# Kernel tuning notes

Hardware: AMD Instinct MI355X
Metric: run time of the kernel (lower is better)

The kernel has to match this reference:

```python
import jax, jax.numpy as jnp
import numpy as np
from jax.ops import segment_sum

N_NODES = 50000
N_EDGES = 800000
IN_DIM, HID_DIM, OUT_DIM = 128, 256, 128


def _glorot(key, shape):
    lim = np.sqrt(6.0 / (shape[0] + shape[1]))
    return jax.random.uniform(key, shape, jnp.float32, -lim, lim)


def setup_inputs() -> dict:
    key = jax.random.key(0)
    ks = jax.random.split(key, 4)
    x = jax.random.normal(ks[0], (N_NODES, IN_DIM), jnp.float32)
    edge_index = jax.random.randint(ks[1], (2, N_EDGES), 0, N_NODES, jnp.int64)
    W1 = _glorot(ks[2], (IN_DIM, HID_DIM))
    b1 = jnp.zeros((HID_DIM,), jnp.float32)
    W2 = _glorot(ks[3], (HID_DIM, OUT_DIM))
    b2 = jnp.zeros((OUT_DIM,), jnp.float32)
    return {"x": x, "edge_index": edge_index, "W1": W1, "b1": b1, "W2": W2, "b2": b2}


def gcn_conv(x, W, b, src, dst, n_nodes):
    # PyG GCNConv: x' = D^{-1/2} (A + I) D^{-1/2} (x W) + b
    h = x @ W  # [N, F_out]
    deg = segment_sum(jnp.ones_like(src, dtype=h.dtype), dst, num_segments=n_nodes) + 1.0  # +1 self loop
    dinv = jax.lax.rsqrt(deg)  # [N]
    norm = dinv[src] * dinv[dst]  # per-edge norm [E]
    msg = h[src] * norm[:, None]  # [E, F_out]
    agg = segment_sum(msg, dst, num_segments=n_nodes)
    agg = agg + h * (dinv * dinv)[:, None]  # self-loop term: norm_ii = dinv_i^2
    return agg + b


def reference(x, edge_index, W1, b1, W2, b2):
    src, dst = edge_index[0], edge_index[1]
    h = gcn_conv(x, W1, b1, src, dst, N_NODES)
    h = jax.nn.relu(h)
    out = gcn_conv(h, W2, b2, src, dst, N_NODES)
    return out
```

## Files before the change

kernel.cpp:

```cpp
#include <hip/hip_runtime.h>

#define N_NODES 50000
#define N_EDGES 800000
#define IN_DIM  128
#define HID_DIM 256
#define OUT_DIM 128
#define BUCKET_CAP 64
#define NCOARSE 196
#define CHUNK 4000
#define NBLK1 200
#define SEGCAP 64
#define AXLD 136

typedef __attribute__((ext_vector_type(8))) short short8;
typedef __attribute__((ext_vector_type(4))) float f32x4;

__device__ inline ushort f2b(float f) {
    union { float f; unsigned u; } v; v.f = f;
    return (ushort)((v.u + 0x7FFFu + ((v.u >> 16) & 1u)) >> 16);
}
__device__ inline float b2f(ushort h) {
    union { unsigned u; float f; } v; v.u = ((unsigned)h) << 16;
    return v.f;
}
__device__ inline float2 u2f2(unsigned u) {
    float2 r; r.x = b2f((ushort)(u & 0xFFFFu)); r.y = b2f((ushort)(u >> 16)); return r;
}
__device__ inline void fma2(float2& a, const float2 v, float n) {
    a.x += v.x * n; a.y += v.y * n;
}


__global__ __launch_bounds__(256) void prep_kernel(const float* __restrict__ x,
                                                   const float* __restrict__ W1,
                                                   const float* __restrict__ W2,
                                                   const int* __restrict__ src,
                                                   const int* __restrict__ dst,
                                                   ushort* __restrict__ xb,
                                                   ushort* __restrict__ w1t,
                                                   ushort* __restrict__ w2t,
                                                   int* __restrict__ bcnt,
                                                   int* __restrict__ binbuf) {
    __shared__ int vals[CHUNK];
    __shared__ ushort lpos[CHUNK];
    __shared__ unsigned char lbin[CHUNK];
    __shared__ int hist[NCOARSE];
    const int b = blockIdx.x;
    const int t = threadIdx.x;
    if (b < 6250) {
        int i = b * 256 + t;
        float4 v = ((const float4*)x)[i];
        ushort4 o; o.x = f2b(v.x); o.y = f2b(v.y); o.z = f2b(v.z); o.w = f2b(v.w);
        ((ushort4*)xb)[i] = o;
    } else if (b < 6506) {
        int i = (b - 6250) * 256 + t;
        if (i < 32768) {
            int n = i >> 7, k = i & 127;
            w1t[i] = f2b(W1[k * HID_DIM + n]);
        } else {
            int j = i - 32768;
            int n = j >> 8, k = j & 255;
            w2t[j] = f2b(W2[k * OUT_DIM + n]);
        }
    } else {
        const int blk = b - 6506;
        const int e0 = blk * CHUNK;
        for (int i = t; i < NCOARSE; i += 256) hist[i] = 0;
        __syncthreads();
        for (int i = t; i < CHUNK; i += 256) {
            int s = src[e0 + i], d = dst[e0 + i];
            int bin = d >> 8;
            vals[i] = (s << 8) | (d & 255);
            lbin[i] = (unsigned char)bin;
            lpos[i] = (ushort)atomicAdd(&hist[bin], 1);
        }
        __syncthreads();
        for (int i = t; i < NCOARSE; i += 256) {
            int h = hist[i]; if (h > SEGCAP) h = SEGCAP;
            bcnt[i * NBLK1 + blk] = h;
        }
        for (int i = t; i < CHUNK; i += 256) {
            int bin = lbin[i];
            int p = lpos[i];
            if (p < SEGCAP) binbuf[((size_t)bin * NBLK1 + blk) * SEGCAP + p] = vals[i];
        }
    }
}


__global__ __launch_bounds__(256) void binpass2_kernel(const int* __restrict__ bcnt,
                                                       const int* __restrict__ binbuf,
                                                       int* __restrict__ cnt,
                                                       float* __restrict__ dinv,
                                                       int* __restrict__ bucket) {
    __shared__ int lcnt[256];
    __shared__ int lm[NBLK1];
    __shared__ int lbuck[256 * BUCKET_CAP];
    const int bin = blockIdx.x;
    const int t = threadIdx.x;
    lcnt[t] = 0;
    if (t < NBLK1) lm[t] = bcnt[bin * NBLK1 + t];
    __syncthreads();
    const int* bb = binbuf + (size_t)bin * NBLK1 * SEGCAP;
    for (int f = t; f < NBLK1 * SEGCAP; f += 256) {
        int blk = f >> 6;
        int sl = f & 63;
        if (sl < lm[blk]) {
            int v = bb[f];
            int dl = v & 255;
            int pos = atomicAdd(&lcnt[dl], 1);
            if (pos < BUCKET_CAP) lbuck[dl * BUCKET_CAP + pos] = v >> 8;
        }
    }
    __syncthreads();
    const int node0 = bin * 256;
    int node = node0 + t;
    if (node < N_NODES) {
        int c = lcnt[t] > BUCKET_CAP ? BUCKET_CAP : lcnt[t];
        cnt[node] = c;
        dinv[node] = rsqrtf((float)c + 1.0f);
    }
    int nvalid = N_NODES - node0; if (nvalid > 256) nvalid = 256;
    if (nvalid <= 0) return;
    int total4 = (nvalid * BUCKET_CAP) >> 2;
    int4* d4 = (int4*)(bucket + (size_t)node0 * BUCKET_CAP);
    const int4* s4 = (const int4*)lbuck;
    for (int j = t; j < total4; j += 256) d4[j] = s4[j];
}


__global__ __launch_bounds__(256) void gg1_kernel(const int* __restrict__ cnt,
                                                  const int* __restrict__ bucket,
                                                  const float* __restrict__ dinv,
                                                  const ushort* __restrict__ xb,
                                                  const ushort* __restrict__ w1t,
                                                  const float* __restrict__ b1,
                                                  ushort* __restrict__ Hb) {
    __shared__ ushort axs[16 * AXLD];
    const int row0 = blockIdx.x * 16;
    const int wv = threadIdx.x >> 6;
    const int lane = threadIdx.x & 63;

    for (int j = 0; j < 4; ++j) {
        const int lr = wv * 4 + j;
        const int node = row0 + lr;
        const int n = cnt[node];
        const float dd = dinv[node];
        int sv = 0; float nv = 0.f;
        if (lane < n) { sv = bucket[node * BUCKET_CAP + lane]; nv = dinv[sv] * dd; }
        float2 self = u2f2(((const unsigned*)(xb + (size_t)node * IN_DIM))[lane]);
        float sd = dd * dd;
        float2 acc[8];
        acc[0] = {self.x * sd, self.y * sd};
#pragma unroll
        for (int k = 1; k < 8; ++k) acc[k] = {0.f, 0.f};
        const int nr = (n + 7) & ~7;
        for (int i = 0; i < nr; i += 8) {
            int s[8]; float nm[8]; unsigned u[8];
#pragma unroll
            for (int k = 0; k < 8; ++k) { s[k] = __shfl(sv, i + k); nm[k] = __shfl(nv, i + k); }
#pragma unroll
            for (int k = 0; k < 8; ++k) u[k] = ((const unsigned*)(xb + (size_t)s[k] * IN_DIM))[lane];
#pragma unroll
            for (int k = 0; k < 8; ++k) fma2(acc[k], u2f2(u[k]), nm[k]);
        }
#pragma unroll
        for (int k = 1; k < 8; ++k) { acc[0].x += acc[k].x; acc[0].y += acc[k].y; }
        unsigned o = (unsigned)f2b(acc[0].x) | ((unsigned)f2b(acc[0].y) << 16);
        ((unsigned*)(axs + lr * AXLD))[lane] = o;
    }
    __syncthreads();

    const int l15 = lane & 15, q = lane >> 4;
    f32x4 acc4[4] = {{0.f, 0.f, 0.f, 0.f}, {0.f, 0.f, 0.f, 0.f},
                     {0.f, 0.f, 0.f, 0.f}, {0.f, 0.f, 0.f, 0.f}};
    const ushort* abase = axs + l15 * AXLD + q * 8;
#pragma unroll
    for (int kb = 0; kb < 4; ++kb) {
        short8 a = *(const short8*)(abase + kb * 32);
#pragma unroll
        for (int t = 0; t < 4; ++t) {
            int col = wv * 64 + t * 16 + l15;
            short8 bfr = *(const short8*)(w1t + (size_t)col * IN_DIM + kb * 32 + q * 8);
            acc4[t] = __builtin_amdgcn_mfma_f32_16x16x32_bf16(a, bfr, acc4[t], 0, 0, 0);
        }
    }
#pragma unroll
    for (int t = 0; t < 4; ++t) {
        int col = wv * 64 + t * 16 + l15;
        float bias = b1[col];
#pragma unroll
        for (int r = 0; r < 4; ++r) {
            int row = row0 + q * 4 + r;
            float v = acc4[t][r] + bias;
            Hb[(size_t)row * HID_DIM + col] = f2b(v > 0.f ? v : 0.f);
        }
    }
}


__global__ __launch_bounds__(256) void gemm2_mfma(const ushort* __restrict__ Hb,
                                                  const ushort* __restrict__ w2t,
                                                  ushort* __restrict__ h2b) {
    const int row0 = blockIdx.x * 16;
    const int wv = threadIdx.x >> 6;
    const int lane = threadIdx.x & 63;
    const int l15 = lane & 15, q = lane >> 4;
    f32x4 acc[2] = {{0.f, 0.f, 0.f, 0.f}, {0.f, 0.f, 0.f, 0.f}};
    const ushort* abase = Hb + (size_t)(row0 + l15) * HID_DIM + q * 8;
#pragma unroll
    for (int kb = 0; kb < 8; ++kb) {
        short8 a = *(const short8*)(abase + kb * 32);
#pragma unroll
        for (int t = 0; t < 2; ++t) {
            int col = wv * 32 + t * 16 + l15;
            short8 b = *(const short8*)(w2t + (size_t)col * HID_DIM + kb * 32 + q * 8);
            acc[t] = __builtin_amdgcn_mfma_f32_16x16x32_bf16(a, b, acc[t], 0, 0, 0);
        }
    }
#pragma unroll
    for (int t = 0; t < 2; ++t) {
        int col = wv * 32 + t * 16 + l15;
#pragma unroll
        for (int r = 0; r < 4; ++r) {
            int row = row0 + q * 4 + r;
            h2b[(size_t)row * OUT_DIM + col] = f2b(acc[t][r]);
        }
    }
}


__global__ __launch_bounds__(256) void gather2_kernel(const int* __restrict__ cnt,
                                                      const int* __restrict__ bucket,
                                                      const float* __restrict__ dinv,
                                                      const ushort* __restrict__ h2b,
                                                      const float* __restrict__ b2,
                                                      float* __restrict__ out) {
    const int w = blockIdx.x * 4 + (threadIdx.x >> 6);
    const int lane = threadIdx.x & 63;
    const int n = cnt[w];
    const float dd = dinv[w];
    int sv = 0; float nv = 0.f;
    if (lane < n) { sv = bucket[w * BUCKET_CAP + lane]; nv = dinv[sv] * dd; }

    float2 bb = ((const float2*)b2)[lane];
    float2 self = u2f2(((const unsigned*)(h2b + (size_t)w * OUT_DIM))[lane]);
    float sd = dd * dd;
    float2 acc[8];
    acc[0] = {self.x * sd + bb.x, self.y * sd + bb.y};
#pragma unroll
    for (int j = 1; j < 8; ++j) acc[j] = {0.f, 0.f};

    const int nr = (n + 7) & ~7;
    for (int i = 0; i < nr; i += 8) {
        int s[8]; float nm[8]; unsigned u[8];
#pragma unroll
        for (int j = 0; j < 8; ++j) { s[j] = __shfl(sv, i + j); nm[j] = __shfl(nv, i + j); }
#pragma unroll
        for (int j = 0; j < 8; ++j) u[j] = ((const unsigned*)(h2b + (size_t)s[j] * OUT_DIM))[lane];
#pragma unroll
        for (int j = 0; j < 8; ++j) fma2(acc[j], u2f2(u[j]), nm[j]);
    }
#pragma unroll
    for (int j = 1; j < 8; ++j) { acc[0].x += acc[j].x; acc[0].y += acc[j].y; }
    ((float2*)(out + (size_t)w * OUT_DIM))[lane] = acc[0];
}

extern "C" void kernel_launch(void* const* d_in, const int* in_sizes, int n_in,
                              void* d_out, int out_size, void* d_ws, size_t ws_size,
                              hipStream_t stream) {
    const float* x  = (const float*)d_in[0];
    const int*   ei = (const int*)d_in[1];
    const float* W1 = (const float*)d_in[2];
    const float* b1 = (const float*)d_in[3];
    const float* W2 = (const float*)d_in[4];
    const float* b2 = (const float*)d_in[5];
    float* out = (float*)d_out;

    const int* src = ei;
    const int* dst = ei + N_EDGES;

    char* ws = (char*)d_ws;
    int*    bcnt   = (int*)(ws);
    int*    cnt    = (int*)(ws + 160000);
    float*  dinv   = (float*)(ws + 360000);
    int*    bucket = (int*)(ws + 560000);
    int*    binbuf = (int*)(ws + 13360000);
    ushort* xb     = (ushort*)(ws + 23395200);
    ushort* w1t    = (ushort*)(ws + 36195200);
    ushort* w2t    = (ushort*)(ws + 36260736);
    ushort* Hb     = (ushort*)(ws + 36326272);
    ushort* h2b    = (ushort*)(ws + 61926272);

    prep_kernel<<<6706, 256, 0, stream>>>(x, W1, W2, src, dst, xb, w1t, w2t, bcnt, binbuf);
    binpass2_kernel<<<NCOARSE, 256, 0, stream>>>(bcnt, binbuf, cnt, dinv, bucket);

    gg1_kernel<<<N_NODES / 16, 256, 0, stream>>>(cnt, bucket, dinv, xb, w1t, b1, Hb);

    gemm2_mfma<<<N_NODES / 16, 256, 0, stream>>>(Hb, w2t, h2b);
    gather2_kernel<<<N_NODES / 4, 256, 0, stream>>>(cnt, bucket, dinv, h2b, b2, out);
}
```

Before: 251.3 us.

## Split layer-1 gather from GEMM, fuse both GEMMs, and widen gather loads

The fused gather+GEMM1 kernel is split into a standalone gather kernel that writes the aggregated bf16 features. A new kernel fuses GEMM1 (with bias and ReLU) and GEMM2, keeping the hidden activations in LDS instead of writing the 256-wide H matrix to global memory and reading it back. Both gather kernels now use 16-byte uint4 loads, with four lane groups each handling a different neighbor, followed by a cross-group shuffle reduction. The cost is an extra global round trip for the 128-wide aggregated input and more shuffle work per edge.

```diff
diff --git a/kernel.cpp b/kernel.cpp
--- a/kernel.cpp
+++ b/kernel.cpp
@@ -10,7 +10,7 @@
 #define CHUNK 4000
 #define NBLK1 200
 #define SEGCAP 64
-#define AXLD 136
+#define HLD 264
 
 typedef __attribute__((ext_vector_type(8))) short short8;
 typedef __attribute__((ext_vector_type(4))) float f32x4;
@@ -26,8 +26,15 @@
 __device__ inline float2 u2f2(unsigned u) {
     float2 r; r.x = b2f((ushort)(u & 0xFFFFu)); r.y = b2f((ushort)(u >> 16)); return r;
 }
-__device__ inline void fma2(float2& a, const float2 v, float n) {
-    a.x += v.x * n; a.y += v.y * n;
+__device__ inline unsigned f2u2(float a, float b) {
+    return (unsigned)f2b(a) | ((unsigned)f2b(b) << 16);
+}
+__device__ inline void fma8(float2* acc, uint4 u, float n) {
+    float2 v0 = u2f2(u.x), v1 = u2f2(u.y), v2 = u2f2(u.z), v3 = u2f2(u.w);
+    acc[0].x += v0.x * n; acc[0].y += v0.y * n;
+    acc[1].x += v1.x * n; acc[1].y += v1.y * n;
+    acc[2].x += v2.x * n; acc[2].y += v2.y * n;
+    acc[3].x += v3.x * n; acc[3].y += v3.y * n;
 }
 
 
@@ -129,93 +136,103 @@
 }
 
 
-__global__ __launch_bounds__(256) void gg1_kernel(const int* __restrict__ cnt,
-                                                  const int* __restrict__ bucket,
-                                                  const float* __restrict__ dinv,
-                                                  const ushort* __restrict__ xb,
-                                                  const ushort* __restrict__ w1t,
-                                                  const float* __restrict__ b1,
-                                                  ushort* __restrict__ Hb) {
-    __shared__ ushort axs[16 * AXLD];
-    const int row0 = blockIdx.x * 16;
-    const int wv = threadIdx.x >> 6;
+__global__ __launch_bounds__(256) void gather0_kernel(const int* __restrict__ cnt,
+                                                      const int* __restrict__ bucket,
+                                                      const float* __restrict__ dinv,
+                                                      const ushort* __restrict__ xb,
+                                                      ushort* __restrict__ aggxb) {
+    const int w = blockIdx.x * 4 + (threadIdx.x >> 6);
     const int lane = threadIdx.x & 63;
-
+    const int grp = lane >> 4, sub = lane & 15;
+    const int n = cnt[w];
+    const float dd = dinv[w];
+    int sv = 0; float nv = 0.f;
+    if (lane < n) { sv = bucket[w * BUCKET_CAP + lane]; nv = dinv[sv] * dd; }
+
+    float2 acc[4];
+    if (grp == 0) {
+        uint4 su = ((const uint4*)(xb + (size_t)w * IN_DIM))[sub];
+        float sd = dd * dd;
+        acc[0] = u2f2(su.x); acc[1] = u2f2(su.y); acc[2] = u2f2(su.z); acc[3] = u2f2(su.w);
+#pragma unroll
+        for (int j = 0; j < 4; ++j) { acc[j].x *= sd; acc[j].y *= sd; }
+    } else {
+#pragma unroll
+        for (int j = 0; j < 4; ++j) acc[j] = {0.f, 0.f};
+    }
+
+    const int nr = (n + 15) & ~15;
+    for (int i = 0; i < nr; i += 16) {
+        int s0 = __shfl(sv, i + grp),      s1 = __shfl(sv, i + 4 + grp);
+        int s2 = __shfl(sv, i + 8 + grp),  s3 = __shfl(sv, i + 12 + grp);
+        float n0 = __shfl(nv, i + grp),     n1 = __shfl(nv, i + 4 + grp);
+        float n2 = __shfl(nv, i + 8 + grp), n3 = __shfl(nv, i + 12 + grp);
+        uint4 u0 = ((const uint4*)(xb + (size_t)s0 * IN_DIM))[sub];
+        uint4 u1 = ((const uint4*)(xb + (size_t)s1 * IN_DIM))[sub];
+        uint4 u2 = ((const uint4*)(xb + (size_t)s2 * IN_DIM))[sub];
+        uint4 u3 = ((const uint4*)(xb + (size_t)s3 * IN_DIM))[sub];
+        fma8(acc, u0, n0); fma8(acc, u1, n1); fma8(acc, u2, n2); fma8(acc, u3, n3);
+    }
+#pragma unroll
     for (int j = 0; j < 4; ++j) {
-        const int lr = wv * 4 + j;
-        const int node = row0 + lr;
-        const int n = cnt[node];
-        const float dd = dinv[node];
-        int sv = 0; float nv = 0.f;
-        if (lane < n) { sv = bucket[node * BUCKET_CAP + lane]; nv = dinv[sv] * dd; }
-        float2 self = u2f2(((const unsigned*)(xb + (size_t)node * IN_DIM))[lane]);
-        float sd = dd * dd;
-        float2 acc[8];
-        acc[0] = {self.x * sd, self.y * sd};
-#pragma unroll
-        for (int k = 1; k < 8; ++k) acc[k] = {0.f, 0.f};
-        const int nr = (n + 7) & ~7;
-        for (int i = 0; i < nr; i += 8) {
-            int s[8]; float nm[8]; unsigned u[8];
-#pragma unroll
-            for (int k = 0; k < 8; ++k) { s[k] = __shfl(sv, i + k); nm[k] = __shfl(nv, i + k); }
-#pragma unroll
-            for (int k = 0; k < 8; ++k) u[k] = ((const unsigned*)(xb + (size_t)s[k] * IN_DIM))[lane];
-#pragma unroll
-            for (int k = 0; k < 8; ++k) fma2(acc[k], u2f2(u[k]), nm[k]);
-        }
-#pragma unroll
-        for (int k = 1; k < 8; ++k) { acc[0].x += acc[k].x; acc[0].y += acc[k].y; }
-        unsigned o = (unsigned)f2b(acc[0].x) | ((unsigned)f2b(acc[0].y) << 16);
-        ((unsigned*)(axs + lr * AXLD))[lane] = o;
-    }
-    __syncthreads();
-
-    const int l15 = lane & 15, q = lane >> 4;
-    f32x4 acc4[4] = {{0.f, 0.f, 0.f, 0.f}, {0.f, 0.f, 0.f, 0.f},
-                     {0.f, 0.f, 0.f, 0.f}, {0.f, 0.f, 0.f, 0.f}};
-    const ushort* abase = axs + l15 * AXLD + q * 8;
-#pragma unroll
-    for (int kb = 0; kb < 4; ++kb) {
-        short8 a = *(const short8*)(abase + kb * 32);
-#pragma unroll
-        for (int t = 0; t < 4; ++t) {
-            int col = wv * 64 + t * 16 + l15;
-            short8 bfr = *(const short8*)(w1t + (size_t)col * IN_DIM + kb * 32 + q * 8);
-            acc4[t] = __builtin_amdgcn_mfma_f32_16x16x32_bf16(a, bfr, acc4[t], 0, 0, 0);
-        }
-    }
-#pragma unroll
-    for (int t = 0; t < 4; ++t) {
-        int col = wv * 64 + t * 16 + l15;
-        float bias = b1[col];
-#pragma unroll
-        for (int r = 0; r < 4; ++r) {
-            int row = row0 + q * 4 + r;
-            float v = acc4[t][r] + bias;
-            Hb[(size_t)row * HID_DIM + col] = f2b(v > 0.f ? v : 0.f);
-        }
-    }
-}
-
-
-__global__ __launch_bounds__(256) void gemm2_mfma(const ushort* __restrict__ Hb,
-                                                  const ushort* __restrict__ w2t,
-                                                  ushort* __restrict__ h2b) {
+        acc[j].x += __shfl_down(acc[j].x, 32); acc[j].y += __shfl_down(acc[j].y, 32);
+        acc[j].x += __shfl_down(acc[j].x, 16); acc[j].y += __shfl_down(acc[j].y, 16);
+    }
+    if (lane < 16) {
+        uint4 o = {f2u2(acc[0].x, acc[0].y), f2u2(acc[1].x, acc[1].y),
+                   f2u2(acc[2].x, acc[2].y), f2u2(acc[3].x, acc[3].y)};
+        ((uint4*)(aggxb + (size_t)w * IN_DIM))[sub] = o;
+    }
+}
+
+
+__global__ __launch_bounds__(256) void gemm12_mfma(const ushort* __restrict__ aggxb,
+                                                   const ushort* __restrict__ w1t,
+                                                   const float* __restrict__ b1,
+                                                   const ushort* __restrict__ w2t,
+                                                   ushort* __restrict__ h2b) {
+    __shared__ ushort Hs[16 * HLD];
     const int row0 = blockIdx.x * 16;
     const int wv = threadIdx.x >> 6;
     const int lane = threadIdx.x & 63;
     const int l15 = lane & 15, q = lane >> 4;
-    f32x4 acc[2] = {{0.f, 0.f, 0.f, 0.f}, {0.f, 0.f, 0.f, 0.f}};
-    const ushort* abase = Hb + (size_t)(row0 + l15) * HID_DIM + q * 8;
+
+    f32x4 acc1[4] = {{0.f, 0.f, 0.f, 0.f}, {0.f, 0.f, 0.f, 0.f},
+                     {0.f, 0.f, 0.f, 0.f}, {0.f, 0.f, 0.f, 0.f}};
+    const ushort* abase = aggxb + (size_t)(row0 + l15) * IN_DIM + q * 8;
+#pragma unroll
+    for (int kb = 0; kb < 4; ++kb) {
+        short8 a = *(const short8*)(abase + kb * 32);
+#pragma unroll
+        for (int t = 0; t < 4; ++t) {
+            int col = wv * 64 + t * 16 + l15;
+            short8 bfr = *(const short8*)(w1t + (size_t)col * IN_DIM + kb * 32 + q * 8);
+            acc1[t] = __builtin_amdgcn_mfma_f32_16x16x32_bf16(a, bfr, acc1[t], 0, 0, 0);
+        }
+    }
+#pragma unroll
+    for (int t = 0; t < 4; ++t) {
+        int col = wv * 64 + t * 16 + l15;
+        float bias = b1[col];
+#pragma unroll
+        for (int r = 0; r < 4; ++r) {
+            int row = q * 4 + r;
+            float v = acc1[t][r] + bias;
+            Hs[row * HLD + col] = f2b(v > 0.f ? v : 0.f);
+        }
+    }
+    __syncthreads();
+
+    f32x4 acc2[2] = {{0.f, 0.f, 0.f, 0.f}, {0.f, 0.f, 0.f, 0.f}};
+    const ushort* hbase = Hs + l15 * HLD + q * 8;
 #pragma unroll
     for (int kb = 0; kb < 8; ++kb) {
-        short8 a = *(const short8*)(abase + kb * 32);
+        short8 a = *(const short8*)(hbase + kb * 32);
 #pragma unroll
         for (int t = 0; t < 2; ++t) {
             int col = wv * 32 + t * 16 + l15;
-            short8 b = *(const short8*)(w2t + (size_t)col * HID_DIM + kb * 32 + q * 8);
-            acc[t] = __builtin_amdgcn_mfma_f32_16x16x32_bf16(a, b, acc[t], 0, 0, 0);
+            short8 bfr = *(const short8*)(w2t + (size_t)col * HID_DIM + kb * 32 + q * 8);
+            acc2[t] = __builtin_amdgcn_mfma_f32_16x16x32_bf16(a, bfr, acc2[t], 0, 0, 0);
         }
     }
 #pragma unroll
@@ -224,7 +241,7 @@
 #pragma unroll
         for (int r = 0; r < 4; ++r) {
             int row = row0 + q * 4 + r;
-            h2b[(size_t)row * OUT_DIM + col] = f2b(acc[t][r]);
+            h2b[(size_t)row * OUT_DIM + col] = f2b(acc2[t][r]);
         }
     }
 }
@@ -238,32 +255,50 @@
                                                       float* __restrict__ out) {
     const int w = blockIdx.x * 4 + (threadIdx.x >> 6);
     const int lane = threadIdx.x & 63;
+    const int grp = lane >> 4, sub = lane & 15;
     const int n = cnt[w];
     const float dd = dinv[w];
     int sv = 0; float nv = 0.f;
     if (lane < n) { sv = bucket[w * BUCKET_CAP + lane]; nv = dinv[sv] * dd; }
 
-    float2 bb = ((const float2*)b2)[lane];
-    float2 self = u2f2(((const unsigned*)(h2b + (size_t)w * OUT_DIM))[lane]);
-    float sd = dd * dd;
-    float2 acc[8];
-    acc[0] = {self.x * sd + bb.x, self.y * sd + bb.y};
-#pragma unroll
-    for (int j = 1; j < 8; ++j) acc[j] = {0.f, 0.f};
-
-    const int nr = (n + 7) & ~7;
-    for (int i = 0; i < nr; i += 8) {
-        int s[8]; float nm[8]; unsigned u[8];
-#pragma unroll
-        for (int j = 0; j < 8; ++j) { s[j] = __shfl(sv, i + j); nm[j] = __shfl(nv, i + j); }
-#pragma unroll
-        for (int j = 0; j < 8; ++j) u[j] = ((const unsigned*)(h2b + (size_t)s[j] * OUT_DIM))[lane];
-#pragma unroll
-        for (int j = 0; j < 8; ++j) fma2(acc[j], u2f2(u[j]), nm[j]);
-    }
-#pragma unroll
-    for (int j = 1; j < 8; ++j) { acc[0].x += acc[j].x; acc[0].y += acc[j].y; }
-    ((float2*)(out + (size_t)w * OUT_DIM))[lane] = acc[0];
+    float2 acc[4];
+    if (grp == 0) {
+        uint4 su = ((const uint4*)(h2b + (size_t)w * OUT_DIM))[sub];
+        float sd = dd * dd;
+        acc[0] = u2f2(su.x); acc[1] = u2f2(su.y); acc[2] = u2f2(su.z); acc[3] = u2f2(su.w);
+#pragma unroll
+        for (int j = 0; j < 4; ++j) { acc[j].x *= sd; acc[j].y *= sd; }
+    } else {
+#pragma unroll
+        for (int j = 0; j < 4; ++j) acc[j] = {0.f, 0.f};
+    }
+
+    const int nr = (n + 15) & ~15;
+    for (int i = 0; i < nr; i += 16) {
+        int s0 = __shfl(sv, i + grp),      s1 = __shfl(sv, i + 4 + grp);
+        int s2 = __shfl(sv, i + 8 + grp),  s3 = __shfl(sv, i + 12 + grp);
+        float n0 = __shfl(nv, i + grp),     n1 = __shfl(nv, i + 4 + grp);
+        float n2 = __shfl(nv, i + 8 + grp), n3 = __shfl(nv, i + 12 + grp);
+        uint4 u0 = ((const uint4*)(h2b + (size_t)s0 * OUT_DIM))[sub];
+        uint4 u1 = ((const uint4*)(h2b + (size_t)s1 * OUT_DIM))[sub];
+        uint4 u2 = ((const uint4*)(h2b + (size_t)s2 * OUT_DIM))[sub];
+        uint4 u3 = ((const uint4*)(h2b + (size_t)s3 * OUT_DIM))[sub];
+        fma8(acc, u0, n0); fma8(acc, u1, n1); fma8(acc, u2, n2); fma8(acc, u3, n3);
+    }
+#pragma unroll
+    for (int j = 0; j < 4; ++j) {
+        acc[j].x += __shfl_down(acc[j].x, 32); acc[j].y += __shfl_down(acc[j].y, 32);
+        acc[j].x += __shfl_down(acc[j].x, 16); acc[j].y += __shfl_down(acc[j].y, 16);
+    }
+    if (lane < 16) {
+        const float4* bp = (const float4*)b2;
+        float4 b0 = bp[sub * 2], b1v = bp[sub * 2 + 1];
+        float4 o0 = {acc[0].x + b0.x, acc[0].y + b0.y, acc[1].x + b0.z, acc[1].y + b0.w};
+        float4 o1 = {acc[2].x + b1v.x, acc[2].y + b1v.y, acc[3].x + b1v.z, acc[3].y + b1v.w};
+        float4* op = (float4*)(out + (size_t)w * OUT_DIM);
+        op[sub * 2] = o0;
+        op[sub * 2 + 1] = o1;
+    }
 }
 
 extern "C" void kernel_launch(void* const* d_in, const int* in_sizes, int n_in,
@@ -289,14 +324,14 @@
     ushort* xb     = (ushort*)(ws + 23395200);
     ushort* w1t    = (ushort*)(ws + 36195200);
     ushort* w2t    = (ushort*)(ws + 36260736);
-    ushort* Hb     = (ushort*)(ws + 36326272);
-    ushort* h2b    = (ushort*)(ws + 61926272);
+    ushort* aggxb  = (ushort*)(ws + 36326272);
+    ushort* h2b    = (ushort*)(ws + 49126272);
 
     prep_kernel<<<6706, 256, 0, stream>>>(x, W1, W2, src, dst, xb, w1t, w2t, bcnt, binbuf);
     binpass2_kernel<<<NCOARSE, 256, 0, stream>>>(bcnt, binbuf, cnt, dinv, bucket);
 
-    gg1_kernel<<<N_NODES / 16, 256, 0, stream>>>(cnt, bucket, dinv, xb, w1t, b1, Hb);
-
-    gemm2_mfma<<<N_NODES / 16, 256, 0, stream>>>(Hb, w2t, h2b);
+    gather0_kernel<<<N_NODES / 4, 256, 0, stream>>>(cnt, bucket, dinv, xb, aggxb);
+    gemm12_mfma<<<N_NODES / 16, 256, 0, stream>>>(aggxb, w1t, b1, w2t, h2b);
+
     gather2_kernel<<<N_NODES / 4, 256, 0, stream>>>(cnt, bucket, dinv, h2b, b2, out);
 }
```

Measured after the change: 244.0 us. 1.03x faster.
